# Optimization experiments

Measured on AMD Instinct MI355X. Metric: run time of the kernel, lower is better.

Reference implementation:

```python
import jax, jax.numpy as jnp
import numpy as np

K_SIZE = 5
PAD = 2  # (dilation*(k-1)+1 - stride + 1)//2 with k=5, dil=1, stride=1
SAMPLE_NUM = 15
DEPTH_MAX = 192.0


def _gather_patches(x, sample_idx):
    """x: [B,C,H,W] -> [B,H,W,S,C]: values of the 5x5 local neighborhood at the
    SAMPLE_NUM sampled kernel positions (zero padding, matching nn.Unfold)."""
    B, C, H, W = x.shape
    xp = jnp.pad(x, ((0, 0), (0, 0), (PAD, PAD), (PAD, PAD)))
    slabs = []
    for i in range(SAMPLE_NUM):  # small fixed constant, not a data dim
        p = sample_idx[i]
        dy = p // K_SIZE
        dx = p % K_SIZE
        slabs.append(jax.lax.dynamic_slice(xp, (0, 0, dy, dx), (B, C, H, W)))
    pat = jnp.stack(slabs, axis=1)          # [B,S,C,H,W]
    return pat.transpose(0, 3, 4, 1, 2)     # [B,H,W,S,C]


def setup_inputs() -> dict:
    key = jax.random.key(0)
    k1, k2, k3, k4 = jax.random.split(key, 4)
    B, C, H, W = 2, 32, 240, 320
    depth = jax.random.uniform(k1, (B, 1, H, W), dtype=jnp.float32) * 200.0
    surface_normal = jax.random.normal(k2, (B, 3, H, W), dtype=jnp.float32)
    features = jax.random.normal(k3, (B, C, H, W), dtype=jnp.float32)
    guide_weight = jnp.ones((B, H, W, K_SIZE * K_SIZE), dtype=jnp.float32)
    sample_idx = jax.random.randint(k4, (SAMPLE_NUM,), 0, K_SIZE * K_SIZE, dtype=jnp.int32)
    return {"depth": depth, "surface_normal": surface_normal, "features": features,
            "guide_weight": guide_weight, "sample_idx": sample_idx}


def reference(depth, surface_normal, features, guide_weight, sample_idx):
    b, c, h, w = features.shape
    d = depth[:, 0]                                          # squeeze(1) -> [B,H,W]
    valid = ((d > 0) & (d < DEPTH_MAX)).astype(features.dtype)[:, None]  # [B,1,H,W]

    feat_s = _gather_patches(features, sample_idx)           # [B,H,W,S,C]
    norm_s = _gather_patches(surface_normal, sample_idx)     # [B,H,W,S,3]
    valid_s = _gather_patches(valid, sample_idx)[..., 0]     # [B,H,W,S]

    # Faithful to torch: surface_normal.view(b, h, w, 3) is a raw memory
    # reinterpretation, NOT a permute.
    center_n = jnp.reshape(surface_normal, (b, h, w, 3))
    diff = jnp.sqrt(jnp.sum((norm_s - center_n[:, :, :, None, :]) ** 2, axis=-1))
    # torch detaches via the cpu/numpy round-trip -> stop_gradient here
    normal_w = jax.lax.stop_gradient(jnp.exp(-0.5 * diff))   # [B,H,W,S]

    guide_s = jnp.take(guide_weight, sample_idx, axis=3)     # [B,H,W,S]

    fw = valid_s * normal_w * guide_s                        # both weight flags True
    fw = jax.nn.softmax(fw, axis=-1)
    out = jnp.sum(feat_s * fw[..., None], axis=3)            # [B,H,W,C]
    return (out.transpose(0, 3, 1, 2), features)
```

## Files before the change

kernel.cpp:

```cpp
#include <hip/hip_runtime.h>

#define K_SIZE 5
#define PAD 2
#define SAMPLE_NUM 15
#define DEPTH_MAX 192.0f

constexpr int B = 2, C = 32, H = 240, W = 320;
constexpr int HW  = H * W;
constexpr int BHW = B * HW;
constexpr int TOT = B * C * HW;
constexpr size_t WS_NEED = (size_t)SAMPLE_NUM * BHW * sizeof(float);

typedef float float4a __attribute__((ext_vector_type(4), aligned(16)));
typedef float float4u __attribute__((ext_vector_type(4), aligned(4)));

__global__ __launch_bounds__(256) void weights_kernel(
    const float* __restrict__ depth,
    const float* __restrict__ sn,
    const float* __restrict__ guide,
    const int*   __restrict__ sample_idx,
    float* __restrict__ wpost)
{
    const int t   = threadIdx.x;
    const int s   = t & 15;
    const int lp  = t >> 4;
    const int pg  = blockIdx.x * 16 + lp;
    const int b   = pg / HW;
    const int pix = pg - b * HW;
    const int y   = pix / W;
    const int x   = pix - y * W;

    const float* snb = sn + (size_t)b * 3 * HW;
    const float* db  = depth + (size_t)b * HW;

    const int pp = sample_idx[(s < SAMPLE_NUM) ? s : 0];
    const int dy = pp / K_SIZE - PAD;
    const int dx = pp - (pp / K_SIZE) * K_SIZE - PAD;
    const int yy = y + dy, xx = x + dx;
    const bool inb = (s < SAMPLE_NUM) && (yy >= 0) && (yy < H) && (xx >= 0) && (xx < W);
    const int  noff = min(max(yy, 0), H - 1) * W + min(max(xx, 0), W - 1);

    const float d  = db[noff];
    const int   o  = pix * 3;
    const float cn0 = snb[o], cn1 = snb[o + 1], cn2 = snb[o + 2];
    const float d0 = snb[noff]          - cn0;
    const float d1 = snb[HW + noff]     - cn1;
    const float d2 = snb[2 * HW + noff] - cn2;
    const float gv = guide[((size_t)b * HW + pix) * 25 + pp];

    const float diff = sqrtf(d0 * d0 + d1 * d1 + d2 * d2);
    const bool  ok   = inb && (d > 0.0f) && (d < DEPTH_MAX);
    const float prew = ok ? __expf(-0.5f * diff) * gv : 0.0f;

    float m = prew;
    #pragma unroll
    for (int mask = 1; mask < 16; mask <<= 1)
        m = fmaxf(m, __shfl_xor(m, mask, 16));
    float e = (s < SAMPLE_NUM) ? __expf(prew - m) : 0.0f;
    float sum = e;
    #pragma unroll
    for (int mask = 1; mask < 16; mask <<= 1)
        sum += __shfl_xor(sum, mask, 16);

    if (s < SAMPLE_NUM)
        wpost[(size_t)s * BHW + pg] = inb ? (e / sum) : 0.0f;
}

constexpr int CHUNKS = BHW / 256;
constexpr int XCHUNK = CHUNKS / 8;

__global__ __launch_bounds__(256, 6) void gather_kernel(
    const float* __restrict__ features,
    const int*   __restrict__ sample_idx,
    const float* __restrict__ wpost,
    float* __restrict__ out,
    float* __restrict__ feat_out)
{
    const int bid   = blockIdx.x;
    const int xcd   = bid & 7;
    const int r     = bid >> 3;
    const int cg    = r / XCHUNK;
    const int chunk = xcd * XCHUNK + (r - (r / XCHUNK) * XCHUNK);

    const int t     = threadIdx.x;
    const int q     = t & 63;
    const int cslot = t >> 6;
    const int c     = cg * 4 + cslot;

    const int p0   = chunk * 256 + q * 4;
    const int b    = p0 / HW;
    const int pix0 = p0 - b * HW;
    const int y    = pix0 / W;
    const int x0   = pix0 - y * W;

    const int fbase = (b * C + c) * HW;

    float4a acc = {0.0f, 0.0f, 0.0f, 0.0f};
    #pragma unroll
    for (int s = 0; s < SAMPLE_NUM; ++s) {
        int pp = sample_idx[s];
        int dy = pp / K_SIZE - PAD;
        int dx = pp - (pp / K_SIZE) * K_SIZE - PAD;
        int yy = min(max(y + dy, 0), H - 1);
        int flat = fbase + yy * W + x0 + dx;
        flat = min(max(flat, 0), TOT - 4);
        float4a w4 = *(const float4a*)(wpost + (size_t)s * BHW + p0);
        float4u f4 = *(const float4u*)(features + flat);
        acc += w4 * f4;
    }

    const bool fix = (fbase == 0 && x0 == 0 && y <= 2) ||
                     (fbase == (B * C - 1) * HW && x0 == W - 4 && y >= H - 3);
    if (fix) {
        const float* fb = features + fbase;
        float a0 = 0, a1 = 0, a2 = 0, a3 = 0;
        #pragma unroll
        for (int s = 0; s < SAMPLE_NUM; ++s) {
            int pp = sample_idx[s];
            int dy = pp / K_SIZE - PAD;
            int dx = pp - (pp / K_SIZE) * K_SIZE - PAD;
            int yy = min(max(y + dy, 0), H - 1);
            const float* frow = fb + yy * W;
            const float* wrow = wpost + (size_t)s * BHW + p0;
            int xb = x0 + dx;
            a0 += wrow[0] * frow[min(max(xb + 0, 0), W - 1)];
            a1 += wrow[1] * frow[min(max(xb + 1, 0), W - 1)];
            a2 += wrow[2] * frow[min(max(xb + 2, 0), W - 1)];
            a3 += wrow[3] * frow[min(max(xb + 3, 0), W - 1)];
        }
        acc = float4a{a0, a1, a2, a3};
    }

    const size_t ob = (size_t)fbase + pix0;
    float4a pf = *(const float4a*)(features + fbase + pix0);
    *(float4a*)(out + ob)      = acc;
    *(float4a*)(feat_out + ob) = pf;
}

__global__ __launch_bounds__(256) void fused_fallback(
    const float* __restrict__ depth, const float* __restrict__ sn,
    const float* __restrict__ features, const float* __restrict__ guide,
    const int* __restrict__ sample_idx, float* __restrict__ out,
    float* __restrict__ feat_out)
{
    constexpr int PIX_BLOCKS = BHW / 256;
    int pb = blockIdx.x % PIX_BLOCKS;
    int g  = blockIdx.x / PIX_BLOCKS;
    int n  = pb * 256 + threadIdx.x;
    int b = n / HW, pix = n - b * HW, y = pix / W, x = pix - y * W;
    const float* snb = sn + (size_t)b * 3 * HW;
    const float* db  = depth + (size_t)b * HW;
    const float* gb  = guide + ((size_t)b * HW + pix) * 25;
    int o = pix * 3;
    float cn0 = snb[o], cn1 = snb[o + 1], cn2 = snb[o + 2];
    float w[SAMPLE_NUM]; int offs[SAMPLE_NUM]; bool inbv[SAMPLE_NUM];
    float m = 0.0f;
    #pragma unroll
    for (int s = 0; s < SAMPLE_NUM; ++s) {
        int pp = sample_idx[s];
        int dy = pp / K_SIZE - PAD, dx = pp - (pp / K_SIZE) * K_SIZE - PAD;
        int yy = y + dy, xx = x + dx;
        bool inb = (yy >= 0) && (yy < H) && (xx >= 0) && (xx < W);
        inbv[s] = inb;
        int noff = inb ? (yy * W + xx) : pix;
        offs[s] = noff;
        float ww = 0.0f;
        if (inb) {
            float d = db[noff];
            if (d > 0.0f && d < DEPTH_MAX) {
                float d0 = snb[noff] - cn0, d1 = snb[HW + noff] - cn1, d2 = snb[2 * HW + noff] - cn2;
                ww = __expf(-0.5f * sqrtf(d0 * d0 + d1 * d1 + d2 * d2)) * gb[pp];
            }
        }
        w[s] = ww; m = fmaxf(m, ww);
    }
    float sum = 0.0f;
    #pragma unroll
    for (int s = 0; s < SAMPLE_NUM; ++s) { w[s] = __expf(w[s] - m); sum += w[s]; }
    float inv = 1.0f / sum;
    #pragma unroll
    for (int s = 0; s < SAMPLE_NUM; ++s) w[s] = inbv[s] ? (w[s] * inv) : 0.0f;
    const float* fb = features + (size_t)b * C * HW;
    float* ob = out + (size_t)b * C * HW;
    float* fob = feat_out + (size_t)b * C * HW;
    int c0 = g * 8;
    #pragma unroll
    for (int cc = 0; cc < 8; ++cc) {
        const float* fc = fb + (c0 + cc) * HW;
        float acc = 0.0f;
        #pragma unroll
        for (int s = 0; s < SAMPLE_NUM; ++s) acc += w[s] * fc[offs[s]];
        ob[(size_t)(c0 + cc) * HW + pix] = acc;
        fob[(size_t)(c0 + cc) * HW + pix] = fc[pix];
    }
}

extern "C" void kernel_launch(void* const* d_in, const int* in_sizes, int n_in,
                              void* d_out, int out_size, void* d_ws, size_t ws_size,
                              hipStream_t stream) {
    const float* depth      = (const float*)d_in[0];
    const float* sn         = (const float*)d_in[1];
    const float* features   = (const float*)d_in[2];
    const float* guide      = (const float*)d_in[3];
    const int*   sample_idx = (const int*)d_in[4];

    float* out      = (float*)d_out;
    float* feat_out = (float*)d_out + (size_t)B * C * HW;

    if (ws_size >= WS_NEED) {
        float* wpost = (float*)d_ws;
        weights_kernel<<<BHW / 16, 256, 0, stream>>>(depth, sn, guide, sample_idx, wpost);
        gather_kernel<<<CHUNKS * 8, 256, 0, stream>>>(features, sample_idx, wpost, out, feat_out);
    } else {
        fused_fallback<<<(BHW / 256) * 4, 256, 0, stream>>>(
            depth, sn, features, guide, sample_idx, out, feat_out);
    }
}
```

Baseline: 47.64 us.

## Store softmax weights pixel-major and gather one pixel per thread

The weights workspace moves from sample-major [S][BHW] to pixel-major [BHW][16], so each gather thread reads its 16 weights with four aligned vector loads. The gather kernel now handles one pixel per thread with scalar feature loads instead of four pixels per thread with unaligned float4 loads, which lets the boundary fix-up path be removed. The grid grows fourfold and the occupancy hint is dropped. In exchange, feature loads are no longer vectorized, the per-pixel weight reads are strided across lanes, and the weights kernel now also writes the padding slot.

```diff
diff --git a/kernel.cpp b/kernel.cpp
--- a/kernel.cpp
+++ b/kernel.cpp
@@ -9,10 +9,9 @@
 constexpr int HW  = H * W;
 constexpr int BHW = B * HW;
 constexpr int TOT = B * C * HW;
-constexpr size_t WS_NEED = (size_t)SAMPLE_NUM * BHW * sizeof(float);
+constexpr size_t WS_NEED = (size_t)BHW * 16 * sizeof(float);
 
 typedef float float4a __attribute__((ext_vector_type(4), aligned(16)));
-typedef float float4u __attribute__((ext_vector_type(4), aligned(4)));
 
 __global__ __launch_bounds__(256) void weights_kernel(
     const float* __restrict__ depth,
@@ -40,13 +39,13 @@
     const bool inb = (s < SAMPLE_NUM) && (yy >= 0) && (yy < H) && (xx >= 0) && (xx < W);
     const int  noff = min(max(yy, 0), H - 1) * W + min(max(xx, 0), W - 1);
 
-    const float d  = db[noff];
-    const int   o  = pix * 3;
+    const float d   = db[noff];
+    const int   o   = pix * 3;
     const float cn0 = snb[o], cn1 = snb[o + 1], cn2 = snb[o + 2];
-    const float d0 = snb[noff]          - cn0;
-    const float d1 = snb[HW + noff]     - cn1;
-    const float d2 = snb[2 * HW + noff] - cn2;
-    const float gv = guide[((size_t)b * HW + pix) * 25 + pp];
+    const float d0  = snb[noff]          - cn0;
+    const float d1  = snb[HW + noff]     - cn1;
+    const float d2  = snb[2 * HW + noff] - cn2;
+    const float gv  = guide[((size_t)b * HW + pix) * 25 + pp];
 
     const float diff = sqrtf(d0 * d0 + d1 * d1 + d2 * d2);
     const bool  ok   = inb && (d > 0.0f) && (d < DEPTH_MAX);
@@ -62,79 +61,59 @@
     for (int mask = 1; mask < 16; mask <<= 1)
         sum += __shfl_xor(sum, mask, 16);
 
-    if (s < SAMPLE_NUM)
-        wpost[(size_t)s * BHW + pg] = inb ? (e / sum) : 0.0f;
+    const float wfin = (s < SAMPLE_NUM && inb) ? (e / sum) : 0.0f;
+    wpost[(size_t)pg * 16 + s] = wfin;
 }
 
-constexpr int CHUNKS = BHW / 256;
+constexpr int CHUNKS = BHW / 64;
 constexpr int XCHUNK = CHUNKS / 8;
 
-__global__ __launch_bounds__(256, 6) void gather_kernel(
+__global__ __launch_bounds__(256) void gather_kernel(
     const float* __restrict__ features,
     const int*   __restrict__ sample_idx,
     const float* __restrict__ wpost,
     float* __restrict__ out,
     float* __restrict__ feat_out)
 {
-    const int bid   = blockIdx.x;
-    const int xcd   = bid & 7;
-    const int r     = bid >> 3;
-    const int cg    = r / XCHUNK;
-    const int chunk = xcd * XCHUNK + (r - (r / XCHUNK) * XCHUNK);
+    const int bid  = blockIdx.x;
+    const int xcd  = bid & 7;
+    const int r    = bid >> 3;
+    const int cg   = r / XCHUNK;
+    const int chnk = xcd * XCHUNK + (r - (r / XCHUNK) * XCHUNK);
 
-    const int t     = threadIdx.x;
-    const int q     = t & 63;
-    const int cslot = t >> 6;
-    const int c     = cg * 4 + cslot;
+    const int lane = threadIdx.x & 63;
+    const int wv   = threadIdx.x >> 6;
+    const int c    = cg * 4 + wv;
 
-    const int p0   = chunk * 256 + q * 4;
-    const int b    = p0 / HW;
-    const int pix0 = p0 - b * HW;
-    const int y    = pix0 / W;
-    const int x0   = pix0 - y * W;
+    const int pg  = chnk * 64 + lane;
+    const int b   = pg / HW;
+    const int pix = pg - b * HW;
+    const int y   = pix / W;
+    const int x   = pix - y * W;
 
-    const int fbase = (b * C + c) * HW;
+    const int plane = (b * C + c) * HW;
 
-    float4a acc = {0.0f, 0.0f, 0.0f, 0.0f};
+    const float4a* wp = (const float4a*)(wpost + (size_t)pg * 16);
+    float4a q0 = wp[0], q1 = wp[1], q2 = wp[2], q3 = wp[3];
+    const float wq[16] = {q0.x, q0.y, q0.z, q0.w, q1.x, q1.y, q1.z, q1.w,
+                          q2.x, q2.y, q2.z, q2.w, q3.x, q3.y, q3.z, q3.w};
+
+    float acc = 0.0f;
     #pragma unroll
     for (int s = 0; s < SAMPLE_NUM; ++s) {
         int pp = sample_idx[s];
         int dy = pp / K_SIZE - PAD;
         int dx = pp - (pp / K_SIZE) * K_SIZE - PAD;
         int yy = min(max(y + dy, 0), H - 1);
-        int flat = fbase + yy * W + x0 + dx;
-        flat = min(max(flat, 0), TOT - 4);
-        float4a w4 = *(const float4a*)(wpost + (size_t)s * BHW + p0);
-        float4u f4 = *(const float4u*)(features + flat);
-        acc += w4 * f4;
+        int flat = plane + yy * W + x + dx;
+        flat = min(max(flat, 0), TOT - 1);
+        acc = fmaf(wq[s], features[flat], acc);
     }
 
-    const bool fix = (fbase == 0 && x0 == 0 && y <= 2) ||
-                     (fbase == (B * C - 1) * HW && x0 == W - 4 && y >= H - 3);
-    if (fix) {
-        const float* fb = features + fbase;
-        float a0 = 0, a1 = 0, a2 = 0, a3 = 0;
-        #pragma unroll
-        for (int s = 0; s < SAMPLE_NUM; ++s) {
-            int pp = sample_idx[s];
-            int dy = pp / K_SIZE - PAD;
-            int dx = pp - (pp / K_SIZE) * K_SIZE - PAD;
-            int yy = min(max(y + dy, 0), H - 1);
-            const float* frow = fb + yy * W;
-            const float* wrow = wpost + (size_t)s * BHW + p0;
-            int xb = x0 + dx;
-            a0 += wrow[0] * frow[min(max(xb + 0, 0), W - 1)];
-            a1 += wrow[1] * frow[min(max(xb + 1, 0), W - 1)];
-            a2 += wrow[2] * frow[min(max(xb + 2, 0), W - 1)];
-            a3 += wrow[3] * frow[min(max(xb + 3, 0), W - 1)];
-        }
-        acc = float4a{a0, a1, a2, a3};
-    }
-
-    const size_t ob = (size_t)fbase + pix0;
-    float4a pf = *(const float4a*)(features + fbase + pix0);
-    *(float4a*)(out + ob)      = acc;
-    *(float4a*)(feat_out + ob) = pf;
+    const int fo = plane + pix;
+    const float pf = features[fo];
+    out[fo]      = acc;
+    feat_out[fo] = pf;
 }
 
 __global__ __launch_bounds__(256) void fused_fallback(
```

Result: slower. 50.80 us (+6.6%).
